# Kernel tuning notes

Hardware: AMD Instinct MI355X
Metric: run time of the kernel (lower is better)

The kernel has to match this reference:

```python
import jax, jax.numpy as jnp
import numpy as np

TOP_K = 2

def setup_inputs() -> dict:
    key = jax.random.key(0)
    k1, k2, k3, k4 = jax.random.split(key, 4)
    T, H, E, I = 2048, 1024, 16, 768
    x = jax.random.normal(k1, (T, H), dtype=jnp.float32)
    gate_w = jax.random.normal(k2, (E, H), dtype=jnp.float32) * 0.02
    w13 = jax.random.normal(k3, (E, 2 * I, H), dtype=jnp.float32) * 0.02
    w2 = jax.random.normal(k4, (E, H, I), dtype=jnp.float32) * 0.02
    return {"x": x, "gate_w": gate_w, "w13": w13, "w2": w2}


def reference(x, gate_w, w13, w2):
    # x: [T, H] tokens; gate_w: [E, H]; w13: [E, 2I, H]; w2: [E, H, I]
    T, H = x.shape
    E = gate_w.shape[0]
    I = w2.shape[-1]

    # --- route: gate matmul + softmax top-k router (renormalize=True) ---
    router_logits = x @ gate_w.T                                  # [T, E]
    probs = jax.nn.softmax(router_logits.astype(jnp.float32), axis=-1)
    topk_w, topk_ids = jax.lax.top_k(probs, TOP_K)                # [T, K]
    topk_w = topk_w / jnp.sum(topk_w, axis=-1, keepdims=True)     # renormalize
    topk_w = topk_w.astype(x.dtype)

    # dense combine weights [T, E]: scatter top-k weights back (dispatch/combine)
    dense_gates = jnp.zeros((T, E), dtype=x.dtype)
    dense_gates = dense_gates.at[jnp.arange(T)[:, None], topk_ids].add(topk_w)

    # --- apply sparse experts: SwiGLU FFN per expert, combined by gates ---
    def expert_step(acc, packed):
        w13_e, w2_e, g_e = packed        # [2I,H], [H,I], [T]
        h = x @ w13_e.T                  # [T, 2I]
        act = jax.nn.silu(h[:, :I]) * h[:, I:]   # gate_proj * up_proj
        return acc + g_e[:, None] * (act @ w2_e.T), None

    acc0 = jnp.zeros_like(x)
    out, _ = jax.lax.scan(expert_step, acc0, (w13, w2, dense_gates.T))
    return out
```

## Files before the change

### kernel.cpp

```cpp
#include <hip/hip_runtime.h>
#include <hip/hip_bf16.h>
#include <hip/hip_fp16.h>
#include <math.h>

#define T_TOK 2048
#define HDIM  1024
#define NEXP  16
#define IDIM  768
#define BM    128
#define MAXROWS 6144

using f16   = _Float16;
using f16x4 = __attribute__((ext_vector_type(4))) _Float16;
using f16x8 = __attribute__((ext_vector_type(8))) _Float16;
using f32x4 = __attribute__((ext_vector_type(4))) float;

__device__ __forceinline__ f16x8 cvt2(float4 a, float4 b) {
    f16x8 r;
    r[0] = (f16)a.x; r[1] = (f16)a.y; r[2] = (f16)a.z; r[3] = (f16)a.w;
    r[4] = (f16)b.x; r[5] = (f16)b.y; r[6] = (f16)b.z; r[7] = (f16)b.w;
    return r;
}

__global__ __launch_bounds__(256) void router_kernel(
    const float* __restrict__ x, const float* __restrict__ gw,
    int* __restrict__ tok_e, float* __restrict__ tok_w, int* __restrict__ cnt)
{
    int wave = threadIdx.x >> 6;
    int lane = threadIdx.x & 63;
    int t = blockIdx.x * 4 + wave;
    if (t >= T_TOK) return;

    const float* xrow = x + (size_t)t * HDIM;
    float xv[16];
#pragma unroll
    for (int j = 0; j < 16; ++j) xv[j] = xrow[lane + 64 * j];

    float logits[NEXP];
#pragma unroll
    for (int e = 0; e < NEXP; ++e) {
        const float* gr = gw + (size_t)e * HDIM;
        float s = 0.f;
#pragma unroll
        for (int j = 0; j < 16; ++j) s += xv[j] * gr[lane + 64 * j];
#pragma unroll
        for (int o = 32; o > 0; o >>= 1) s += __shfl_xor(s, o, 64);
        logits[e] = s;
    }

    int i1 = 0; float m1 = logits[0];
#pragma unroll
    for (int e = 1; e < NEXP; ++e) if (logits[e] > m1) { m1 = logits[e]; i1 = e; }
    int i2 = -1; float m2 = -3.0e38f;
#pragma unroll
    for (int e = 0; e < NEXP; ++e) if (e != i1 && logits[e] > m2) { m2 = logits[e]; i2 = e; }

    float w1 = 1.f / (1.f + expf(m2 - m1));
    float w2 = 1.f - w1;

    if (lane == 0) {
        tok_e[t * 2 + 0] = i1; tok_e[t * 2 + 1] = i2;
        tok_w[t * 2 + 0] = w1; tok_w[t * 2 + 1] = w2;
        atomicAdd(&cnt[i1], 1);
        atomicAdd(&cnt[i2], 1);
    }
}

__global__ void prefix_kernel(const int* __restrict__ cnt, int* __restrict__ base,
                              int* __restrict__ total)
{
    if (threadIdx.x == 0) {
        int b = 0;
        for (int e = 0; e < NEXP; ++e) {
            base[e] = b;
            b += (cnt[e] + BM - 1) & ~(BM - 1);
        }
        base[NEXP] = b;
        *total = b;
    }
}

__global__ __launch_bounds__(256) void scatter_kernel(
    const int* __restrict__ tok_e, const float* __restrict__ tok_w,
    const int* __restrict__ base, int* __restrict__ cnt2,
    int* __restrict__ rowslot, float* __restrict__ rowgate)
{
    int t = blockIdx.x * 256 + threadIdx.x;
    if (t >= T_TOK) return;
#pragma unroll
    for (int k = 0; k < 2; ++k) {
        int e = tok_e[t * 2 + k];
        int pos = atomicAdd(&cnt2[e], 1);
        int row = base[e] + pos;
        rowslot[row] = t * 2 + k;
        rowgate[row] = tok_w[t * 2 + k];
    }
}

__global__ __launch_bounds__(256) void gemm1_kernel(
    const float* __restrict__ x, const float* __restrict__ w13,
    const int* __restrict__ rowslot, const int* __restrict__ base,
    const int* __restrict__ cnt, const int* __restrict__ total,
    f16* __restrict__ act)
{
    int row0 = blockIdx.x * BM;
    if (row0 >= *total) return;
    int nt = blockIdx.y;

    int e = 0;
#pragma unroll
    for (int i = 1; i < NEXP; ++i) if (base[i] <= row0) e = i;
    int basee = base[e], cnte = cnt[e];

    __shared__ f16 a_sm[128 * 40];
    __shared__ f16 b_sm[128 * 40];

    int tid = threadIdx.x;
    int srow = tid >> 1;
    int scol = (tid & 1) * 16;

    bool avalid = (unsigned)(row0 + srow - basee) < (unsigned)cnte;
    const float* aptr = x;
    if (avalid) {
        int tok = rowslot[row0 + srow] >> 1;
        aptr = x + (size_t)tok * HDIM + scol;
    }

    int wrow = (srow < 64) ? (nt * 64 + srow) : (IDIM + nt * 64 + (srow - 64));
    const float* bptr = w13 + (size_t)e * 2 * IDIM * HDIM + (size_t)wrow * HDIM + scol;

    int wv = tid >> 6, lane = tid & 63, l16 = lane & 15, lk = lane >> 4;
    f32x4 acc[2][8] = {};

    for (int k0 = 0; k0 < HDIM; k0 += 32) {
        __syncthreads();
        {
            float4 a0{0,0,0,0}, a1{0,0,0,0}, a2{0,0,0,0}, a3{0,0,0,0};
            if (avalid) {
                a0 = *(const float4*)(aptr + k0);
                a1 = *(const float4*)(aptr + k0 + 4);
                a2 = *(const float4*)(aptr + k0 + 8);
                a3 = *(const float4*)(aptr + k0 + 12);
            }
            float4 b0 = *(const float4*)(bptr + k0);
            float4 b1 = *(const float4*)(bptr + k0 + 4);
            float4 b2 = *(const float4*)(bptr + k0 + 8);
            float4 b3 = *(const float4*)(bptr + k0 + 12);
            *(f16x8*)&a_sm[srow * 40 + scol]     = cvt2(a0, a1);
            *(f16x8*)&a_sm[srow * 40 + scol + 8] = cvt2(a2, a3);
            *(f16x8*)&b_sm[srow * 40 + scol]     = cvt2(b0, b1);
            *(f16x8*)&b_sm[srow * 40 + scol + 8] = cvt2(b2, b3);
        }
        __syncthreads();

        f16x8 af[2], bf[8];
#pragma unroll
        for (int m = 0; m < 2; ++m)
            af[m] = *(const f16x8*)&a_sm[(wv * 32 + m * 16 + l16) * 40 + lk * 8];
#pragma unroll
        for (int n = 0; n < 8; ++n)
            bf[n] = *(const f16x8*)&b_sm[(n * 16 + l16) * 40 + lk * 8];
#pragma unroll
        for (int m = 0; m < 2; ++m)
#pragma unroll
            for (int n = 0; n < 8; ++n)
                acc[m][n] = __builtin_amdgcn_mfma_f32_16x16x32_f16(af[m], bf[n], acc[m][n], 0, 0, 0);
    }

#pragma unroll
    for (int m = 0; m < 2; ++m)
#pragma unroll
        for (int n = 0; n < 4; ++n)
#pragma unroll
            for (int j = 0; j < 4; ++j) {
                float hg = acc[m][n][j];
                float hu = acc[m][n + 4][j];
                float s = hg / (1.f + expf(-hg));
                int row = row0 + wv * 32 + m * 16 + lk * 4 + j;
                act[(size_t)row * IDIM + nt * 64 + n * 16 + l16] = (f16)(s * hu);
            }
}

__global__ __launch_bounds__(256) void gemm2_kernel(
    const f16* __restrict__ act, const float* __restrict__ w2,
    const int* __restrict__ rowslot, const float* __restrict__ rowgate,
    const int* __restrict__ base, const int* __restrict__ cnt, const int* __restrict__ total,
    float* __restrict__ out)
{
    int row0 = blockIdx.x * BM;
    if (row0 >= *total) return;
    int nt = blockIdx.y;

    int e = 0;
#pragma unroll
    for (int i = 1; i < NEXP; ++i) if (base[i] <= row0) e = i;
    int basee = base[e], cnte = cnt[e];

    __shared__ f16 a_sm[128 * 40];
    __shared__ f16 b_sm[128 * 40];

    int tid = threadIdx.x;
    int srow = tid >> 1;
    int scol = (tid & 1) * 16;

    const f16*   aptr = act + (size_t)(row0 + srow) * IDIM + scol;
    const float* bptr = w2 + (size_t)e * HDIM * IDIM + (size_t)(nt * 128 + srow) * IDIM + scol;

    int wv = tid >> 6, lane = tid & 63, l16 = lane & 15, lk = lane >> 4;
    f32x4 acc[2][8] = {};

    for (int k0 = 0; k0 < IDIM; k0 += 32) {
        __syncthreads();
        {
            f16x8 alo = *(const f16x8*)(aptr + k0);
            f16x8 ahi = *(const f16x8*)(aptr + k0 + 8);
            float4 b0 = *(const float4*)(bptr + k0);
            float4 b1 = *(const float4*)(bptr + k0 + 4);
            float4 b2 = *(const float4*)(bptr + k0 + 8);
            float4 b3 = *(const float4*)(bptr + k0 + 12);
            *(f16x8*)&a_sm[srow * 40 + scol]     = alo;
            *(f16x8*)&a_sm[srow * 40 + scol + 8] = ahi;
            *(f16x8*)&b_sm[srow * 40 + scol]     = cvt2(b0, b1);
            *(f16x8*)&b_sm[srow * 40 + scol + 8] = cvt2(b2, b3);
        }
        __syncthreads();

        f16x8 af[2], bf[8];
#pragma unroll
        for (int m = 0; m < 2; ++m)
            af[m] = *(const f16x8*)&a_sm[(wv * 32 + m * 16 + l16) * 40 + lk * 8];
#pragma unroll
        for (int n = 0; n < 8; ++n)
            bf[n] = *(const f16x8*)&b_sm[(n * 16 + l16) * 40 + lk * 8];
#pragma unroll
        for (int m = 0; m < 2; ++m)
#pragma unroll
            for (int n = 0; n < 8; ++n)
                acc[m][n] = __builtin_amdgcn_mfma_f32_16x16x32_f16(af[m], bf[n], acc[m][n], 0, 0, 0);
    }

#pragma unroll
    for (int m = 0; m < 2; ++m)
#pragma unroll
        for (int j = 0; j < 4; ++j) {
            int row = row0 + wv * 32 + m * 16 + lk * 4 + j;
            if ((unsigned)(row - basee) < (unsigned)cnte) {
                int s = rowslot[row];
                float g = rowgate[row];
                float* orow = out + (size_t)(s >> 1) * HDIM + nt * 128;
#pragma unroll
                for (int n = 0; n < 8; ++n)
                    atomicAdd(&orow[n * 16 + l16], g * acc[m][n][j]);
            }
        }
}

extern "C" void kernel_launch(void* const* d_in, const int* in_sizes, int n_in,
                              void* d_out, int out_size, void* d_ws, size_t ws_size,
                              hipStream_t stream) {
    const float* x   = (const float*)d_in[0];
    const float* gw  = (const float*)d_in[1];
    const float* w13 = (const float*)d_in[2];
    const float* w2  = (const float*)d_in[3];
    float* out = (float*)d_out;

    char* ws = (char*)d_ws;
    size_t off = 0;
    f16* act       = (f16*)(ws + off);   off += (size_t)MAXROWS * IDIM * 2;
    int* rowslot   = (int*)(ws + off);   off += (size_t)MAXROWS * 4;
    float* rowgate = (float*)(ws + off); off += (size_t)MAXROWS * 4;
    int* tok_e     = (int*)(ws + off);   off += (size_t)T_TOK * 2 * 4;
    float* tok_w   = (float*)(ws + off); off += (size_t)T_TOK * 2 * 4;
    int* cnt       = (int*)(ws + off);   off += 64;
    int* cnt2      = (int*)(ws + off);   off += 64;
    int* base      = (int*)(ws + off);   off += 128;
    int* total     = (int*)(ws + off);   off += 64;

    hipMemsetAsync(cnt, 0, 128, stream);
    hipMemsetAsync(out, 0, (size_t)T_TOK * HDIM * 4, stream);

    router_kernel<<<T_TOK / 4, 256, 0, stream>>>(x, gw, tok_e, tok_w, cnt);
    prefix_kernel<<<1, 64, 0, stream>>>(cnt, base, total);
    scatter_kernel<<<T_TOK / 256, 256, 0, stream>>>(tok_e, tok_w, base, cnt2, rowslot, rowgate);

    dim3 g1(MAXROWS / BM, (2 * IDIM) / 128);
    gemm1_kernel<<<g1, 256, 0, stream>>>(x, w13, rowslot, base, cnt, total, act);

    dim3 g2(MAXROWS / BM, HDIM / 128);
    gemm2_kernel<<<g2, 256, 0, stream>>>(act, w2, rowslot, rowgate, base, cnt, total, out);
}
```

Measured before the change: 353.3 us.

## Add register prefetch pipelining, BK=64, and narrower N tiles to MoE GEMMs

Both expert GEMMs now prefetch the next K tile from global memory into registers while MFMAs run on the current LDS tile. The K step doubles to 64, which halves the number of barrier pairs. The N tile shrinks from 128 to 64 columns, doubling the grid, and launch bounds request 3 blocks per CU for more occupancy. In exchange, each A row is reloaded from global memory twice as often, and register pressure from the prefetch buffers may limit occupancy.

```diff
diff --git a/kernel.cpp b/kernel.cpp
--- a/kernel.cpp
+++ b/kernel.cpp
@@ -8,6 +8,8 @@
 #define NEXP  16
 #define IDIM  768
 #define BM    128
+#define BK    64
+#define LDA   72
 #define MAXROWS 6144
 
 using f16   = _Float16;
@@ -97,7 +99,7 @@
     }
 }
 
-__global__ __launch_bounds__(256) void gemm1_kernel(
+__global__ __launch_bounds__(256, 3) void gemm1_kernel(
     const float* __restrict__ x, const float* __restrict__ w13,
     const int* __restrict__ rowslot, const int* __restrict__ base,
     const int* __restrict__ cnt, const int* __restrict__ total,
@@ -112,76 +114,87 @@
     for (int i = 1; i < NEXP; ++i) if (base[i] <= row0) e = i;
     int basee = base[e], cnte = cnt[e];
 
-    __shared__ f16 a_sm[128 * 40];
-    __shared__ f16 b_sm[128 * 40];
+    __shared__ f16 a_sm[128 * LDA];
+    __shared__ f16 b_sm[64 * LDA];
 
     int tid = threadIdx.x;
-    int srow = tid >> 1;
-    int scol = (tid & 1) * 16;
-
-    bool avalid = (unsigned)(row0 + srow - basee) < (unsigned)cnte;
+    int srowA = tid >> 1, scolA = (tid & 1) * 32;
+    bool avalid = (unsigned)(row0 + srowA - basee) < (unsigned)cnte;
     const float* aptr = x;
     if (avalid) {
-        int tok = rowslot[row0 + srow] >> 1;
-        aptr = x + (size_t)tok * HDIM + scol;
-    }
-
-    int wrow = (srow < 64) ? (nt * 64 + srow) : (IDIM + nt * 64 + (srow - 64));
-    const float* bptr = w13 + (size_t)e * 2 * IDIM * HDIM + (size_t)wrow * HDIM + scol;
+        int tok = rowslot[row0 + srowA] >> 1;
+        aptr = x + (size_t)tok * HDIM + scolA;
+    }
+    int srowB = tid >> 2, scolB = (tid & 3) * 16;
+    int wrow = (srowB < 32) ? (nt * 32 + srowB) : (IDIM + nt * 32 + (srowB - 32));
+    const float* bptr = w13 + (size_t)e * 2 * IDIM * HDIM + (size_t)wrow * HDIM + scolB;
 
     int wv = tid >> 6, lane = tid & 63, l16 = lane & 15, lk = lane >> 4;
-    f32x4 acc[2][8] = {};
-
-    for (int k0 = 0; k0 < HDIM; k0 += 32) {
+    f32x4 acc[2][4] = {};
+    float4 apre[8], bpre[4];
+
+    auto load_pre = [&](int k0) {
+        if (avalid) {
+#pragma unroll
+            for (int i = 0; i < 8; ++i) apre[i] = *(const float4*)(aptr + k0 + i * 4);
+        } else {
+#pragma unroll
+            for (int i = 0; i < 8; ++i) apre[i] = float4{0.f, 0.f, 0.f, 0.f};
+        }
+#pragma unroll
+        for (int i = 0; i < 4; ++i) bpre[i] = *(const float4*)(bptr + k0 + i * 4);
+    };
+    auto write_lds = [&]() {
+#pragma unroll
+        for (int i = 0; i < 4; ++i)
+            *(f16x8*)&a_sm[srowA * LDA + scolA + i * 8] = cvt2(apre[2 * i], apre[2 * i + 1]);
+#pragma unroll
+        for (int i = 0; i < 2; ++i)
+            *(f16x8*)&b_sm[srowB * LDA + scolB + i * 8] = cvt2(bpre[2 * i], bpre[2 * i + 1]);
+    };
+
+    load_pre(0);
+    write_lds();
+    __syncthreads();
+
+    const int KT = HDIM / BK;
+    for (int t = 0; t < KT; ++t) {
+        if (t + 1 < KT) load_pre((t + 1) * BK);
+#pragma unroll
+        for (int ks = 0; ks < 2; ++ks) {
+            f16x8 af[2], bf[4];
+#pragma unroll
+            for (int m = 0; m < 2; ++m)
+                af[m] = *(const f16x8*)&a_sm[(wv * 32 + m * 16 + l16) * LDA + ks * 32 + lk * 8];
+#pragma unroll
+            for (int n = 0; n < 4; ++n)
+                bf[n] = *(const f16x8*)&b_sm[(n * 16 + l16) * LDA + ks * 32 + lk * 8];
+#pragma unroll
+            for (int m = 0; m < 2; ++m)
+#pragma unroll
+                for (int n = 0; n < 4; ++n)
+                    acc[m][n] = __builtin_amdgcn_mfma_f32_16x16x32_f16(af[m], bf[n], acc[m][n], 0, 0, 0);
+        }
         __syncthreads();
-        {
-            float4 a0{0,0,0,0}, a1{0,0,0,0}, a2{0,0,0,0}, a3{0,0,0,0};
-            if (avalid) {
-                a0 = *(const float4*)(aptr + k0);
-                a1 = *(const float4*)(aptr + k0 + 4);
-                a2 = *(const float4*)(aptr + k0 + 8);
-                a3 = *(const float4*)(aptr + k0 + 12);
-            }
-            float4 b0 = *(const float4*)(bptr + k0);
-            float4 b1 = *(const float4*)(bptr + k0 + 4);
-            float4 b2 = *(const float4*)(bptr + k0 + 8);
-            float4 b3 = *(const float4*)(bptr + k0 + 12);
-            *(f16x8*)&a_sm[srow * 40 + scol]     = cvt2(a0, a1);
-            *(f16x8*)&a_sm[srow * 40 + scol + 8] = cvt2(a2, a3);
-            *(f16x8*)&b_sm[srow * 40 + scol]     = cvt2(b0, b1);
-            *(f16x8*)&b_sm[srow * 40 + scol + 8] = cvt2(b2, b3);
-        }
+        if (t + 1 < KT) write_lds();
         __syncthreads();
-
-        f16x8 af[2], bf[8];
-#pragma unroll
-        for (int m = 0; m < 2; ++m)
-            af[m] = *(const f16x8*)&a_sm[(wv * 32 + m * 16 + l16) * 40 + lk * 8];
-#pragma unroll
-        for (int n = 0; n < 8; ++n)
-            bf[n] = *(const f16x8*)&b_sm[(n * 16 + l16) * 40 + lk * 8];
-#pragma unroll
-        for (int m = 0; m < 2; ++m)
-#pragma unroll
-            for (int n = 0; n < 8; ++n)
-                acc[m][n] = __builtin_amdgcn_mfma_f32_16x16x32_f16(af[m], bf[n], acc[m][n], 0, 0, 0);
     }
 
 #pragma unroll
     for (int m = 0; m < 2; ++m)
 #pragma unroll
-        for (int n = 0; n < 4; ++n)
+        for (int n = 0; n < 2; ++n)
 #pragma unroll
             for (int j = 0; j < 4; ++j) {
                 float hg = acc[m][n][j];
-                float hu = acc[m][n + 4][j];
+                float hu = acc[m][n + 2][j];
                 float s = hg / (1.f + expf(-hg));
                 int row = row0 + wv * 32 + m * 16 + lk * 4 + j;
-                act[(size_t)row * IDIM + nt * 64 + n * 16 + l16] = (f16)(s * hu);
+                act[(size_t)row * IDIM + nt * 32 + n * 16 + l16] = (f16)(s * hu);
             }
 }
 
-__global__ __launch_bounds__(256) void gemm2_kernel(
+__global__ __launch_bounds__(256, 3) void gemm2_kernel(
     const f16* __restrict__ act, const float* __restrict__ w2,
     const int* __restrict__ rowslot, const float* __restrict__ rowgate,
     const int* __restrict__ base, const int* __restrict__ cnt, const int* __restrict__ total,
@@ -196,47 +209,59 @@
     for (int i = 1; i < NEXP; ++i) if (base[i] <= row0) e = i;
     int basee = base[e], cnte = cnt[e];
 
-    __shared__ f16 a_sm[128 * 40];
-    __shared__ f16 b_sm[128 * 40];
+    __shared__ f16 a_sm[128 * LDA];
+    __shared__ f16 b_sm[64 * LDA];
 
     int tid = threadIdx.x;
-    int srow = tid >> 1;
-    int scol = (tid & 1) * 16;
-
-    const f16*   aptr = act + (size_t)(row0 + srow) * IDIM + scol;
-    const float* bptr = w2 + (size_t)e * HDIM * IDIM + (size_t)(nt * 128 + srow) * IDIM + scol;
+    int srowA = tid >> 1, scolA = (tid & 1) * 32;
+    const f16* aptr = act + (size_t)(row0 + srowA) * IDIM + scolA;
+    int srowB = tid >> 2, scolB = (tid & 3) * 16;
+    const float* bptr = w2 + (size_t)e * HDIM * IDIM + (size_t)(nt * 64 + srowB) * IDIM + scolB;
 
     int wv = tid >> 6, lane = tid & 63, l16 = lane & 15, lk = lane >> 4;
-    f32x4 acc[2][8] = {};
-
-    for (int k0 = 0; k0 < IDIM; k0 += 32) {
+    f32x4 acc[2][4] = {};
+    f16x8 apre[4]; float4 bpre[4];
+
+    auto load_pre = [&](int k0) {
+#pragma unroll
+        for (int i = 0; i < 4; ++i) apre[i] = *(const f16x8*)(aptr + k0 + i * 8);
+#pragma unroll
+        for (int i = 0; i < 4; ++i) bpre[i] = *(const float4*)(bptr + k0 + i * 4);
+    };
+    auto write_lds = [&]() {
+#pragma unroll
+        for (int i = 0; i < 4; ++i)
+            *(f16x8*)&a_sm[srowA * LDA + scolA + i * 8] = apre[i];
+#pragma unroll
+        for (int i = 0; i < 2; ++i)
+            *(f16x8*)&b_sm[srowB * LDA + scolB + i * 8] = cvt2(bpre[2 * i], bpre[2 * i + 1]);
+    };
+
+    load_pre(0);
+    write_lds();
+    __syncthreads();
+
+    const int KT = IDIM / BK;
+    for (int t = 0; t < KT; ++t) {
+        if (t + 1 < KT) load_pre((t + 1) * BK);
+#pragma unroll
+        for (int ks = 0; ks < 2; ++ks) {
+            f16x8 af[2], bf[4];
+#pragma unroll
+            for (int m = 0; m < 2; ++m)
+                af[m] = *(const f16x8*)&a_sm[(wv * 32 + m * 16 + l16) * LDA + ks * 32 + lk * 8];
+#pragma unroll
+            for (int n = 0; n < 4; ++n)
+                bf[n] = *(const f16x8*)&b_sm[(n * 16 + l16) * LDA + ks * 32 + lk * 8];
+#pragma unroll
+            for (int m = 0; m < 2; ++m)
+#pragma unroll
+                for (int n = 0; n < 4; ++n)
+                    acc[m][n] = __builtin_amdgcn_mfma_f32_16x16x32_f16(af[m], bf[n], acc[m][n], 0, 0, 0);
+        }
         __syncthreads();
-        {
-            f16x8 alo = *(const f16x8*)(aptr + k0);
-            f16x8 ahi = *(const f16x8*)(aptr + k0 + 8);
-            float4 b0 = *(const float4*)(bptr + k0);
-            float4 b1 = *(const float4*)(bptr + k0 + 4);
-            float4 b2 = *(const float4*)(bptr + k0 + 8);
-            float4 b3 = *(const float4*)(bptr + k0 + 12);
-            *(f16x8*)&a_sm[srow * 40 + scol]     = alo;
-            *(f16x8*)&a_sm[srow * 40 + scol + 8] = ahi;
-            *(f16x8*)&b_sm[srow * 40 + scol]     = cvt2(b0, b1);
-            *(f16x8*)&b_sm[srow * 40 + scol + 8] = cvt2(b2, b3);
-        }
+        if (t + 1 < KT) write_lds();
         __syncthreads();
-
-        f16x8 af[2], bf[8];
-#pragma unroll
-        for (int m = 0; m < 2; ++m)
-            af[m] = *(const f16x8*)&a_sm[(wv * 32 + m * 16 + l16) * 40 + lk * 8];
-#pragma unroll
-        for (int n = 0; n < 8; ++n)
-            bf[n] = *(const f16x8*)&b_sm[(n * 16 + l16) * 40 + lk * 8];
-#pragma unroll
-        for (int m = 0; m < 2; ++m)
-#pragma unroll
-            for (int n = 0; n < 8; ++n)
-                acc[m][n] = __builtin_amdgcn_mfma_f32_16x16x32_f16(af[m], bf[n], acc[m][n], 0, 0, 0);
     }
 
 #pragma unroll
@@ -247,9 +272,9 @@
             if ((unsigned)(row - basee) < (unsigned)cnte) {
                 int s = rowslot[row];
                 float g = rowgate[row];
-                float* orow = out + (size_t)(s >> 1) * HDIM + nt * 128;
-#pragma unroll
-                for (int n = 0; n < 8; ++n)
+                float* orow = out + (size_t)(s >> 1) * HDIM + nt * 64;
+#pragma unroll
+                for (int n = 0; n < 4; ++n)
                     atomicAdd(&orow[n * 16 + l16], g * acc[m][n][j]);
             }
         }
@@ -283,9 +308,9 @@
     prefix_kernel<<<1, 64, 0, stream>>>(cnt, base, total);
     scatter_kernel<<<T_TOK / 256, 256, 0, stream>>>(tok_e, tok_w, base, cnt2, rowslot, rowgate);
 
-    dim3 g1(MAXROWS / BM, (2 * IDIM) / 128);
+    dim3 g1(MAXROWS / BM, IDIM / 32);
     gemm1_kernel<<<g1, 256, 0, stream>>>(x, w13, rowslot, base, cnt, total, act);
 
-    dim3 g2(MAXROWS / BM, HDIM / 128);
+    dim3 g2(MAXROWS / BM, HDIM / 64);
     gemm2_kernel<<<g2, 256, 0, stream>>>(act, w2, rowslot, rowgate, base, cnt, total, out);
 }
```

Result: slower. 386.9 us (+9.5%).

## Pre-cast weights and gathered tokens to fp16, use direct-to-LDS loads in GEMMs

Applied to the files above, without the earlier changes.

Adds a kernel that converts all expert weights to fp16 and a kernel that gathers routed token rows into a packed fp16 buffer. The two GEMMs then load tiles straight into shared memory with global_load_lds, use 512-thread blocks with BK=64, and reorder blocks with a swizzle for cache locality. This removes per-tile fp32-to-fp16 conversion and the indirect gather from the GEMM inner loops. In exchange, every call pays an extra full pass over the fp32 weights plus extra workspace traffic.

```diff
diff --git a/kernel.cpp b/kernel.cpp
--- a/kernel.cpp
+++ b/kernel.cpp
@@ -1,5 +1,4 @@
 #include <hip/hip_runtime.h>
-#include <hip/hip_bf16.h>
 #include <hip/hip_fp16.h>
 #include <math.h>
 
@@ -8,10 +7,14 @@
 #define NEXP  16
 #define IDIM  768
 #define BM    128
+#define BK    64
 #define MAXROWS 6144
 
+#define NW13  (NEXP * 2 * IDIM * HDIM)
+#define NW2   (NEXP * HDIM * IDIM)
+#define NWTOT (NW13 + NW2)
+
 using f16   = _Float16;
-using f16x4 = __attribute__((ext_vector_type(4))) _Float16;
 using f16x8 = __attribute__((ext_vector_type(8))) _Float16;
 using f32x4 = __attribute__((ext_vector_type(4))) float;
 
@@ -20,6 +23,13 @@
     r[0] = (f16)a.x; r[1] = (f16)a.y; r[2] = (f16)a.z; r[3] = (f16)a.w;
     r[4] = (f16)b.x; r[5] = (f16)b.y; r[6] = (f16)b.z; r[7] = (f16)b.w;
     return r;
+}
+
+__device__ __forceinline__ void gload16(const f16* g, f16* l) {
+    __builtin_amdgcn_global_load_lds(
+        (const __attribute__((address_space(1))) unsigned int*)g,
+        (__attribute__((address_space(3))) unsigned int*)l,
+        16, 0, 0);
 }
 
 __global__ __launch_bounds__(256) void router_kernel(
@@ -97,159 +107,186 @@
     }
 }
 
-__global__ __launch_bounds__(256) void gemm1_kernel(
-    const float* __restrict__ x, const float* __restrict__ w13,
-    const int* __restrict__ rowslot, const int* __restrict__ base,
-    const int* __restrict__ cnt, const int* __restrict__ total,
+__global__ __launch_bounds__(256) void wcast_kernel(
+    const float* __restrict__ w13, const float* __restrict__ w2,
+    f16* __restrict__ w13h, f16* __restrict__ w2h)
+{
+    size_t stride = (size_t)gridDim.x * 256 * 8;
+    for (size_t i8 = ((size_t)blockIdx.x * 256 + threadIdx.x) * 8; i8 < (size_t)NWTOT; i8 += stride) {
+        const float* src; f16* dst; size_t off;
+        if (i8 < (size_t)NW13) { src = w13; dst = w13h; off = i8; }
+        else                   { src = w2;  dst = w2h;  off = i8 - NW13; }
+        float4 a = *(const float4*)(src + off);
+        float4 b = *(const float4*)(src + off + 4);
+        *(f16x8*)(dst + off) = cvt2(a, b);
+    }
+}
+
+__global__ __launch_bounds__(256) void xpack_kernel(
+    const float* __restrict__ x, const int* __restrict__ rowslot,
+    const int* __restrict__ base, const int* __restrict__ cnt,
+    f16* __restrict__ xg)
+{
+    int gid = blockIdx.x * 256 + threadIdx.x;
+    int row = gid >> 7, c8 = (gid & 127) * 8;
+    int e = 0;
+#pragma unroll
+    for (int i = 1; i < NEXP; ++i) if (base[i] <= row) e = i;
+    f16x8 o = {};
+    if ((unsigned)(row - base[e]) < (unsigned)cnt[e]) {
+        int tok = rowslot[row] >> 1;
+        const float* p = x + (size_t)tok * HDIM + c8;
+        o = cvt2(*(const float4*)p, *(const float4*)(p + 4));
+    }
+    *(f16x8*)&xg[(size_t)row * HDIM + c8] = o;
+}
+
+__global__ __launch_bounds__(512, 4) void gemm1_kernel(
+    const f16* __restrict__ xg, const f16* __restrict__ w13h,
+    const int* __restrict__ base, const int* __restrict__ total,
     f16* __restrict__ act)
 {
-    int row0 = blockIdx.x * BM;
+    int lin = blockIdx.x + blockIdx.y * 12;
+    int swz = (lin % 8) * 72 + (lin / 8);
+    int chunk = swz / 12;
+    int mb = (chunk % 6) * 8 + (chunk / 6);
+    int nt = swz % 12;
+
+    int row0 = mb * BM;
     if (row0 >= *total) return;
-    int nt = blockIdx.y;
 
     int e = 0;
 #pragma unroll
     for (int i = 1; i < NEXP; ++i) if (base[i] <= row0) e = i;
-    int basee = base[e], cnte = cnt[e];
-
-    __shared__ f16 a_sm[128 * 40];
-    __shared__ f16 b_sm[128 * 40];
+
+    __shared__ f16 a_sm[128 * 64];
+    __shared__ f16 b_sm[128 * 64];
 
     int tid = threadIdx.x;
-    int srow = tid >> 1;
-    int scol = (tid & 1) * 16;
-
-    bool avalid = (unsigned)(row0 + srow - basee) < (unsigned)cnte;
-    const float* aptr = x;
-    if (avalid) {
-        int tok = rowslot[row0 + srow] >> 1;
-        aptr = x + (size_t)tok * HDIM + scol;
-    }
-
-    int wrow = (srow < 64) ? (nt * 64 + srow) : (IDIM + nt * 64 + (srow - 64));
-    const float* bptr = w13 + (size_t)e * 2 * IDIM * HDIM + (size_t)wrow * HDIM + scol;
+    int r0 = tid >> 3;
+    int cg = (tid & 7) * 8;
+
+    const f16* ga0 = xg + (size_t)(row0 + r0) * HDIM + cg;
+    const f16* ga1 = xg + (size_t)(row0 + 64 + r0) * HDIM + cg;
+    const f16* wbase = w13h + (size_t)e * 2 * IDIM * HDIM;
+    const f16* gb0 = wbase + (size_t)(nt * 64 + r0) * HDIM + cg;
+    const f16* gb1 = wbase + (size_t)(IDIM + nt * 64 + r0) * HDIM + cg;
 
     int wv = tid >> 6, lane = tid & 63, l16 = lane & 15, lk = lane >> 4;
-    f32x4 acc[2][8] = {};
-
-    for (int k0 = 0; k0 < HDIM; k0 += 32) {
+    int wr = wv >> 1;
+    int wc = wv & 1;
+
+    f32x4 acc[2][4] = {};
+
+    for (int k0 = 0; k0 < HDIM; k0 += BK) {
         __syncthreads();
-        {
-            float4 a0{0,0,0,0}, a1{0,0,0,0}, a2{0,0,0,0}, a3{0,0,0,0};
-            if (avalid) {
-                a0 = *(const float4*)(aptr + k0);
-                a1 = *(const float4*)(aptr + k0 + 4);
-                a2 = *(const float4*)(aptr + k0 + 8);
-                a3 = *(const float4*)(aptr + k0 + 12);
+        gload16(ga0 + k0, &a_sm[tid * 8]);
+        gload16(ga1 + k0, &a_sm[4096 + tid * 8]);
+        gload16(gb0 + k0, &b_sm[tid * 8]);
+        gload16(gb1 + k0, &b_sm[4096 + tid * 8]);
+        __syncthreads();
+#pragma unroll
+        for (int ks = 0; ks < 2; ++ks) {
+            f16x8 af[2], bf[4];
+#pragma unroll
+            for (int m = 0; m < 2; ++m)
+                af[m] = *(const f16x8*)&a_sm[(wr * 32 + m * 16 + l16) * 64 + ks * 32 + lk * 8];
+#pragma unroll
+            for (int n = 0; n < 2; ++n) {
+                bf[n]     = *(const f16x8*)&b_sm[(wc * 32 + n * 16 + l16) * 64 + ks * 32 + lk * 8];
+                bf[n + 2] = *(const f16x8*)&b_sm[(64 + wc * 32 + n * 16 + l16) * 64 + ks * 32 + lk * 8];
             }
-            float4 b0 = *(const float4*)(bptr + k0);
-            float4 b1 = *(const float4*)(bptr + k0 + 4);
-            float4 b2 = *(const float4*)(bptr + k0 + 8);
-            float4 b3 = *(const float4*)(bptr + k0 + 12);
-            *(f16x8*)&a_sm[srow * 40 + scol]     = cvt2(a0, a1);
-            *(f16x8*)&a_sm[srow * 40 + scol + 8] = cvt2(a2, a3);
-            *(f16x8*)&b_sm[srow * 40 + scol]     = cvt2(b0, b1);
-            *(f16x8*)&b_sm[srow * 40 + scol + 8] = cvt2(b2, b3);
+#pragma unroll
+            for (int m = 0; m < 2; ++m)
+#pragma unroll
+                for (int n = 0; n < 4; ++n)
+                    acc[m][n] = __builtin_amdgcn_mfma_f32_16x16x32_f16(af[m], bf[n], acc[m][n], 0, 0, 0);
         }
-        __syncthreads();
-
-        f16x8 af[2], bf[8];
-#pragma unroll
-        for (int m = 0; m < 2; ++m)
-            af[m] = *(const f16x8*)&a_sm[(wv * 32 + m * 16 + l16) * 40 + lk * 8];
-#pragma unroll
-        for (int n = 0; n < 8; ++n)
-            bf[n] = *(const f16x8*)&b_sm[(n * 16 + l16) * 40 + lk * 8];
-#pragma unroll
-        for (int m = 0; m < 2; ++m)
-#pragma unroll
-            for (int n = 0; n < 8; ++n)
-                acc[m][n] = __builtin_amdgcn_mfma_f32_16x16x32_f16(af[m], bf[n], acc[m][n], 0, 0, 0);
     }
 
 #pragma unroll
     for (int m = 0; m < 2; ++m)
 #pragma unroll
-        for (int n = 0; n < 4; ++n)
+        for (int n = 0; n < 2; ++n)
 #pragma unroll
             for (int j = 0; j < 4; ++j) {
                 float hg = acc[m][n][j];
-                float hu = acc[m][n + 4][j];
-                float s = hg / (1.f + expf(-hg));
-                int row = row0 + wv * 32 + m * 16 + lk * 4 + j;
-                act[(size_t)row * IDIM + nt * 64 + n * 16 + l16] = (f16)(s * hu);
+                float hu = acc[m][n + 2][j];
+                float sg = hg / (1.f + expf(-hg));
+                int row = row0 + wr * 32 + m * 16 + lk * 4 + j;
+                act[(size_t)row * IDIM + nt * 64 + wc * 32 + n * 16 + l16] = (f16)(sg * hu);
             }
 }
 
-__global__ __launch_bounds__(256) void gemm2_kernel(
-    const f16* __restrict__ act, const float* __restrict__ w2,
+__global__ __launch_bounds__(512, 4) void gemm2_kernel(
+    const f16* __restrict__ act, const f16* __restrict__ w2h,
     const int* __restrict__ rowslot, const float* __restrict__ rowgate,
     const int* __restrict__ base, const int* __restrict__ cnt, const int* __restrict__ total,
     float* __restrict__ out)
 {
-    int row0 = blockIdx.x * BM;
+    int lin = blockIdx.x + blockIdx.y * 16;
+    int swz = (lin % 8) * 96 + (lin / 8);
+    int chunk = swz / 16;
+    int mb = (chunk % 6) * 8 + (chunk / 6);
+    int nt = swz % 16;
+
+    int row0 = mb * BM;
     if (row0 >= *total) return;
-    int nt = blockIdx.y;
 
     int e = 0;
 #pragma unroll
     for (int i = 1; i < NEXP; ++i) if (base[i] <= row0) e = i;
     int basee = base[e], cnte = cnt[e];
 
-    __shared__ f16 a_sm[128 * 40];
-    __shared__ f16 b_sm[128 * 40];
+    __shared__ f16 a_sm[128 * 64];
+    __shared__ f16 b_sm[64 * 64];
 
     int tid = threadIdx.x;
-    int srow = tid >> 1;
-    int scol = (tid & 1) * 16;
-
-    const f16*   aptr = act + (size_t)(row0 + srow) * IDIM + scol;
-    const float* bptr = w2 + (size_t)e * HDIM * IDIM + (size_t)(nt * 128 + srow) * IDIM + scol;
+    int r0 = tid >> 3, cg = (tid & 7) * 8;
+
+    const f16* ga0 = act + (size_t)(row0 + r0) * IDIM + cg;
+    const f16* ga1 = act + (size_t)(row0 + 64 + r0) * IDIM + cg;
+    const f16* gb0 = w2h + (size_t)e * HDIM * IDIM + (size_t)(nt * 64 + r0) * IDIM + cg;
 
     int wv = tid >> 6, lane = tid & 63, l16 = lane & 15, lk = lane >> 4;
-    f32x4 acc[2][8] = {};
-
-    for (int k0 = 0; k0 < IDIM; k0 += 32) {
+    int wr = wv >> 1, wc = wv & 1;
+
+    f32x4 acc[2][2] = {};
+
+    for (int k0 = 0; k0 < IDIM; k0 += BK) {
         __syncthreads();
-        {
-            f16x8 alo = *(const f16x8*)(aptr + k0);
-            f16x8 ahi = *(const f16x8*)(aptr + k0 + 8);
-            float4 b0 = *(const float4*)(bptr + k0);
-            float4 b1 = *(const float4*)(bptr + k0 + 4);
-            float4 b2 = *(const float4*)(bptr + k0 + 8);
-            float4 b3 = *(const float4*)(bptr + k0 + 12);
-            *(f16x8*)&a_sm[srow * 40 + scol]     = alo;
-            *(f16x8*)&a_sm[srow * 40 + scol + 8] = ahi;
-            *(f16x8*)&b_sm[srow * 40 + scol]     = cvt2(b0, b1);
-            *(f16x8*)&b_sm[srow * 40 + scol + 8] = cvt2(b2, b3);
+        gload16(ga0 + k0, &a_sm[tid * 8]);
+        gload16(ga1 + k0, &a_sm[4096 + tid * 8]);
+        gload16(gb0 + k0, &b_sm[tid * 8]);
+        __syncthreads();
+#pragma unroll
+        for (int ks = 0; ks < 2; ++ks) {
+            f16x8 af[2], bf[2];
+#pragma unroll
+            for (int m = 0; m < 2; ++m)
+                af[m] = *(const f16x8*)&a_sm[(wr * 32 + m * 16 + l16) * 64 + ks * 32 + lk * 8];
+#pragma unroll
+            for (int n = 0; n < 2; ++n)
+                bf[n] = *(const f16x8*)&b_sm[(wc * 32 + n * 16 + l16) * 64 + ks * 32 + lk * 8];
+#pragma unroll
+            for (int m = 0; m < 2; ++m)
+#pragma unroll
+                for (int n = 0; n < 2; ++n)
+                    acc[m][n] = __builtin_amdgcn_mfma_f32_16x16x32_f16(af[m], bf[n], acc[m][n], 0, 0, 0);
         }
-        __syncthreads();
-
-        f16x8 af[2], bf[8];
-#pragma unroll
-        for (int m = 0; m < 2; ++m)
-            af[m] = *(const f16x8*)&a_sm[(wv * 32 + m * 16 + l16) * 40 + lk * 8];
-#pragma unroll
-        for (int n = 0; n < 8; ++n)
-            bf[n] = *(const f16x8*)&b_sm[(n * 16 + l16) * 40 + lk * 8];
-#pragma unroll
-        for (int m = 0; m < 2; ++m)
-#pragma unroll
-            for (int n = 0; n < 8; ++n)
-                acc[m][n] = __builtin_amdgcn_mfma_f32_16x16x32_f16(af[m], bf[n], acc[m][n], 0, 0, 0);
     }
 
 #pragma unroll
     for (int m = 0; m < 2; ++m)
 #pragma unroll
         for (int j = 0; j < 4; ++j) {
-            int row = row0 + wv * 32 + m * 16 + lk * 4 + j;
+            int row = row0 + wr * 32 + m * 16 + lk * 4 + j;
             if ((unsigned)(row - basee) < (unsigned)cnte) {
-                int s = rowslot[row];
+                int sl = rowslot[row];
                 float g = rowgate[row];
-                float* orow = out + (size_t)(s >> 1) * HDIM + nt * 128;
-#pragma unroll
-                for (int n = 0; n < 8; ++n)
+                float* orow = out + (size_t)(sl >> 1) * HDIM + nt * 64 + wc * 32;
+#pragma unroll
+                for (int n = 0; n < 2; ++n)
                     atomicAdd(&orow[n * 16 + l16], g * acc[m][n][j]);
             }
         }
@@ -266,6 +303,9 @@
 
     char* ws = (char*)d_ws;
     size_t off = 0;
+    f16* w13h      = (f16*)(ws + off);   off += (size_t)NW13 * 2;
+    f16* w2h       = (f16*)(ws + off);   off += (size_t)NW2 * 2;
+    f16* xg        = (f16*)(ws + off);   off += (size_t)MAXROWS * HDIM * 2;
     f16* act       = (f16*)(ws + off);   off += (size_t)MAXROWS * IDIM * 2;
     int* rowslot   = (int*)(ws + off);   off += (size_t)MAXROWS * 4;
     float* rowgate = (float*)(ws + off); off += (size_t)MAXROWS * 4;
@@ -283,9 +323,12 @@
     prefix_kernel<<<1, 64, 0, stream>>>(cnt, base, total);
     scatter_kernel<<<T_TOK / 256, 256, 0, stream>>>(tok_e, tok_w, base, cnt2, rowslot, rowgate);
 
-    dim3 g1(MAXROWS / BM, (2 * IDIM) / 128);
-    gemm1_kernel<<<g1, 256, 0, stream>>>(x, w13, rowslot, base, cnt, total, act);
-
-    dim3 g2(MAXROWS / BM, HDIM / 128);
-    gemm2_kernel<<<g2, 256, 0, stream>>>(act, w2, rowslot, rowgate, base, cnt, total, out);
-}
+    wcast_kernel<<<2048, 256, 0, stream>>>(w13, w2, w13h, w2h);
+    xpack_kernel<<<(MAXROWS * 128) / 256, 256, 0, stream>>>(x, rowslot, base, cnt, xg);
+
+    dim3 g1(12, 48);
+    gemm1_kernel<<<g1, 512, 0, stream>>>(xg, w13h, base, total, act);
+
+    dim3 g2(16, 48);
+    gemm2_kernel<<<g2, 512, 0, stream>>>(act, w2h, rowslot, rowgate, base, cnt, total, out);
+}
```

After: 349.8 us. About the same (-1.0%).
